# Optimization experiments

Measured on AMD Instinct MI355X. Metric: run time of the kernel, lower is better.

The kernel has to match this reference:

```python
import jax, jax.numpy as jnp
import numpy as np
import math

B, S, D, H = 2, 2048, 1024, 32
HD = D // H  # head_dim = 32
NEG = -1e9


def setup_inputs() -> dict:
    key = jax.random.key(0)
    ks = jax.random.split(key, 6)
    x = jax.random.normal(ks[0], (B, S, D), dtype=jnp.float32)
    # additive causal mask: 0 on/below diagonal, -1e9 above
    causal = jnp.tril(jnp.ones((S, S), dtype=bool))
    mask = jnp.where(causal, 0.0, NEG).astype(jnp.float32)[None, None]
    # SSMax-style per-query-position log-length scale
    section_log_len = jnp.log(jnp.arange(1, S + 1, dtype=jnp.float32) + 1.0).reshape(1, 1, S, 1)
    sc = 1.0 / math.sqrt(D)
    wq = jax.random.normal(ks[1], (D, D), dtype=jnp.float32) * sc
    wk = jax.random.normal(ks[2], (D, D), dtype=jnp.float32) * sc
    wv = jax.random.normal(ks[3], (D, D), dtype=jnp.float32) * sc
    wo = jax.random.normal(ks[4], (D, D), dtype=jnp.float32) * sc
    seq_scale = jnp.ones((1, H, 1, 1), dtype=jnp.float32)
    return {"x": x, "mask": mask, "section_log_len": section_log_len,
            "wq": wq, "wk": wk, "wv": wv, "wo": wo, "seq_scale": seq_scale}


def reference(x, mask, section_log_len, wq, wk, wv, wo, seq_scale):
    bsz, seqlen, dim = x.shape
    # projections (torch Linear: y = x @ W.T); split heads -> [b, h, s, hd]
    q = (x @ wq.T).reshape(bsz, seqlen, H, HD).transpose(0, 2, 1, 3)
    k = (x @ wk.T).reshape(bsz, seqlen, H, HD).transpose(0, 2, 1, 3)
    v = (x @ wv.T).reshape(bsz, seqlen, H, HD).transpose(0, 2, 1, 3)
    # n_kv_heads == n_heads, so repeat_kv is identity
    scores = jnp.einsum('bhqd,bhkd->bhqk', q, k) / math.sqrt(HD)
    scores = scores * (section_log_len * seq_scale)  # SSMax per-head learned scale
    scores = scores + mask
    probs = jax.nn.softmax(scores.astype(jnp.float32), axis=-1).astype(q.dtype)
    out = jnp.einsum('bhqk,bhkd->bhqd', probs, v)
    out = out.transpose(0, 2, 1, 3).reshape(bsz, seqlen, dim)
    return out @ wo.T
```

## Files before the change

### kernel.cpp

```cpp
#include <hip/hip_runtime.h>
#include <hip/hip_bf16.h>

typedef __bf16 bf16_t;
typedef bf16_t bf16x8 __attribute__((ext_vector_type(8)));
typedef float f32x4 __attribute__((ext_vector_type(4)));

#define NB 2
#define SEQ 2048
#define DIM 1024
#define NH 32
#define HDIM 32

#define LDA 40

static __device__ __forceinline__ f32x4 mfma16(bf16x8 a, bf16x8 b, f32x4 c) {
    return __builtin_amdgcn_mfma_f32_16x16x32_bf16(a, b, c, 0, 0, 0);
}

static __device__ __forceinline__ float fexp2(float x) {
    float r;
    asm("v_exp_f32 %0, %1" : "=v"(r) : "v"(x));
    return r;
}

static __device__ __forceinline__ void load_lds16(const bf16_t* g, bf16_t* l) {
    __builtin_amdgcn_global_load_lds(
        (const __attribute__((address_space(1))) void*)(g),
        (__attribute__((address_space(3))) void*)(l), 16, 0, 0);
}

__global__ __launch_bounds__(256)
void cvt_f32_bf16(const float* __restrict__ s0, bf16_t* __restrict__ d0, int n0,
                  const float* __restrict__ s1, bf16_t* __restrict__ d1, int n1,
                  const float* __restrict__ s2, bf16_t* __restrict__ d2, int n2,
                  const float* __restrict__ s3, bf16_t* __restrict__ d3, int n3,
                  const float* __restrict__ s4, bf16_t* __restrict__ d4, int n4) {
    const int stride = gridDim.x * blockDim.x;
    const int tid = blockIdx.x * blockDim.x + threadIdx.x;
    const float* src[5] = {s0, s1, s2, s3, s4};
    bf16_t* dst[5] = {d0, d1, d2, d3, d4};
    const int n[5] = {n0, n1, n2, n3, n4};
#pragma unroll
    for (int r = 0; r < 5; r++) {
        const int nv = n[r] >> 2;
        for (int i = tid; i < nv; i += stride) {
            float4 v = ((const float4*)src[r])[i];
            bf16_t o[4] = {(bf16_t)v.x, (bf16_t)v.y, (bf16_t)v.z, (bf16_t)v.w};
            *(uint2*)(dst[r] + i * 4) = *(const uint2*)o;
        }
    }
}

template <int EPI, int BM>
__global__ __launch_bounds__(256)
void gemm_pipe(const bf16_t* __restrict__ A, const bf16_t* __restrict__ W,
               float* __restrict__ Cf, bf16_t* __restrict__ qb,
               bf16_t* __restrict__ kb, bf16_t* __restrict__ vtb,
               const float* __restrict__ slen, const float* __restrict__ ss) {
    constexpr int MI = BM / 32;
    constexpr int ABUF = BM * 32;
    __shared__ alignas(16) bf16_t As[3 * ABUF];
    __shared__ alignas(16) bf16_t Bs[3 * 4096];
    const int t = threadIdx.x;
    const int lane = t & 63, wave = t >> 6;
    const int lane16 = lane & 15, quad = lane >> 4;
    const int wm = (wave >> 1) * (BM / 2), wn = (wave & 1) * 64;
    const int id = blockIdx.x;
    int m0, n0g;
    if (EPI == 1) {
        const int xcd = id & 7, slot = id >> 3;
        m0 = (xcd + 8 * (slot & 3)) * 128;
        n0g = (slot >> 2) * 128;
    } else {
        const int xcd = id & 7, slot = id >> 3;
        m0 = (xcd + 8 * (slot & 7)) * 64;
        n0g = (slot >> 3) * 128;
    }
    const int tr = t >> 2;
    const int tc = ((t & 3) ^ ((tr >> 1) & 3)) * 8;
    const bf16_t* ga = A + (m0 + tr) * DIM + tc;
    const bf16_t* gb = W + (n0g + tr) * DIM + tc;
    const int rq = (quad ^ ((lane16 >> 1) & 3)) * 8;
    const bool vseg = (EPI == 1) && (n0g >= 2048);

    f32x4 acc[MI][4];
#pragma unroll
    for (int i = 0; i < MI; i++)
#pragma unroll
        for (int j = 0; j < 4; j++) acc[i][j] = f32x4{0.f, 0.f, 0.f, 0.f};

    auto stage = [&](int k0, int buf) {
        bf16_t* a_dst = As + buf * ABUF + (t & 192) * 8;
        bf16_t* b_dst = Bs + buf * 4096 + (t & 192) * 8;
        load_lds16(ga + k0, a_dst);
        if (BM == 128) load_lds16(ga + 64 * DIM + k0, a_dst + 2048);
        load_lds16(gb + k0, b_dst);
        load_lds16(gb + 64 * DIM + k0, b_dst + 2048);
    };
    auto compute = [&](int buf) {
        bf16x8 af[MI], bfr[4];
#pragma unroll
        for (int mi = 0; mi < MI; mi++)
            af[mi] = *(const bf16x8*)(As + buf * ABUF +
                                      (wm + mi * 16 + lane16) * 32 + rq);
#pragma unroll
        for (int ni = 0; ni < 4; ni++)
            bfr[ni] = *(const bf16x8*)(Bs + buf * 4096 +
                                       (wn + ni * 16 + lane16) * 32 + rq);
        if (vseg) {
#pragma unroll
            for (int mi = 0; mi < MI; mi++)
#pragma unroll
                for (int ni = 0; ni < 4; ni++)
                    acc[mi][ni] = mfma16(bfr[ni], af[mi], acc[mi][ni]);
        } else {
#pragma unroll
            for (int mi = 0; mi < MI; mi++)
#pragma unroll
                for (int ni = 0; ni < 4; ni++)
                    acc[mi][ni] = mfma16(af[mi], bfr[ni], acc[mi][ni]);
        }
    };

    stage(0, 0);
    stage(32, 1);
#pragma unroll
    for (int k0 = 0; k0 < DIM; k0 += 32) {
        const int it = k0 >> 5;
        const int cur = it % 3;
        if (k0 + 64 < DIM) {
            stage(k0 + 64, (it + 2) % 3);
            if (BM == 128)
                asm volatile("s_waitcnt vmcnt(8)" ::: "memory");
            else
                asm volatile("s_waitcnt vmcnt(6)" ::: "memory");
        } else if (k0 + 32 < DIM) {
            if (BM == 128)
                asm volatile("s_waitcnt vmcnt(4)" ::: "memory");
            else
                asm volatile("s_waitcnt vmcnt(3)" ::: "memory");
        } else {
            asm volatile("s_waitcnt vmcnt(0)" ::: "memory");
        }
        asm volatile("s_barrier" ::: "memory");
        compute(cur);
        if (k0 + 32 < DIM) {
            asm volatile("s_waitcnt lgkmcnt(0)" ::: "memory");
            asm volatile("s_barrier" ::: "memory");
        }
    }

    if (EPI == 0) {
#pragma unroll
        for (int mi = 0; mi < MI; mi++)
#pragma unroll
            for (int ni = 0; ni < 4; ni++)
#pragma unroll
                for (int r = 0; r < 4; r++) {
                    int row = m0 + wm + mi * 16 + quad * 4 + r;
                    int col = n0g + wn + ni * 16 + lane16;
                    Cf[row * DIM + col] = acc[mi][ni][r];
                }
    } else if (!vseg) {
        const bool isq = (n0g < 1024);
        bf16_t* dst = isq ? qb : kb;
        const int nb = n0g & 1023;
#pragma unroll
        for (int mi = 0; mi < MI; mi++)
#pragma unroll
            for (int ni = 0; ni < 4; ni++) {
                const int h = ((nb + wn) >> 5) + (ni >> 1);
                const float hscale =
                    isq ? ss[h] * (0.17677669529663687f * 1.4426950408889634f)
                        : 0.f;
#pragma unroll
                for (int r = 0; r < 4; r++) {
                    int m = m0 + wm + mi * 16 + quad * 4 + r;
                    int nl = nb + wn + ni * 16 + lane16;
                    int b = m >> 11, s = m & (SEQ - 1);
                    int d = nl & 31;
                    float v = acc[mi][ni][r];
                    if (isq) v *= slen[s] * hscale;
                    dst[(((b * NH + h) << 11) + s) * 32 + d] = (bf16_t)v;
                }
            }
    } else {
        const int nb = n0g & 1023;
#pragma unroll
        for (int mi = 0; mi < MI; mi++)
#pragma unroll
            for (int ni = 0; ni < 4; ni++)
#pragma unroll
                for (int r = 0; r < 4; r++) {
                    int nl = nb + wn + ni * 16 + quad * 4 + r;
                    int m = m0 + wm + mi * 16 + lane16;
                    int b = m >> 11, s = m & (SEQ - 1);
                    int h = nl >> 5, d = nl & 31;
                    vtb[(((b * NH + h) << 5) + d) * SEQ + s] = (bf16_t)acc[mi][ni][r];
                }
    }
}

__global__ __launch_bounds__(256)
void attn_fwd(const bf16_t* __restrict__ q, const bf16_t* __restrict__ k,
              const bf16_t* __restrict__ vt, bf16_t* __restrict__ out) {
    __shared__ alignas(16) bf16_t pscr[4][2][32 * LDA];
    const int t = threadIdx.x;
    const int lane = t & 63, wave = t >> 6;
    const int lane16 = lane & 15, quad = lane >> 4;
    const int gw = blockIdx.x * 4 + wave;
    const int idx = gw & 63;
    const int qt = (idx & 1) ? (63 - (idx >> 1)) : (idx >> 1);
    const int h = (gw >> 6) & (NH - 1);
    const int b = gw >> 11;
    const int q0 = qt * 32;
    const bf16_t* qh = q + (b * NH + h) * SEQ * HDIM;
    const bf16_t* kh = k + (b * NH + h) * SEQ * HDIM;
    const bf16_t* vth = vt + (b * NH + h) * HDIM * SEQ;

    bf16_t* wbase0 = pscr[wave][0] + quad * 4 * LDA + 2 * lane16;
    bf16_t* wbase1 = pscr[wave][1] + quad * 4 * LDA + 2 * lane16;
    const bf16_t* rbase0 = pscr[wave][0] + lane16 * LDA + quad * 8;
    const bf16_t* rbase1 = pscr[wave][1] + lane16 * LDA + quad * 8;

    bf16x8 qf[2];
    qf[0] = *(const bf16x8*)(qh + (q0 + lane16) * HDIM + quad * 8);
    qf[1] = *(const bf16x8*)(qh + (q0 + 16 + lane16) * HDIM + quad * 8);

    bf16x8 ones;
#pragma unroll
    for (int j = 0; j < 8; j++) ones[j] = (bf16_t)1.0f;

    f32x4 o[2][2], ol[2], sc[2][2];
#pragma unroll
    for (int mi = 0; mi < 2; mi++) {
        ol[mi] = f32x4{0.f, 0.f, 0.f, 0.f};
#pragma unroll
        for (int ni = 0; ni < 2; ni++) o[mi][ni] = f32x4{0.f, 0.f, 0.f, 0.f};
    }

    const bf16_t* kp0 = kh + (2 * lane16) * HDIM + quad * 8;
    const bf16_t* vp0 = vth + lane16 * SEQ + quad * 8;
    const bf16_t* vp1 = vth + (16 + lane16) * SEQ + quad * 8;

    const f32x4 zz = f32x4{0.f, 0.f, 0.f, 0.f};
    bf16x8 kc0, kc1, pf0, pf1, vprev0, vprev1;

    auto qk = [&]() {
        __builtin_amdgcn_s_setprio(1);
        sc[0][0] = mfma16(qf[0], kc0, zz);
        sc[0][1] = mfma16(qf[0], kc1, zz);
        sc[1][0] = mfma16(qf[1], kc0, zz);
        sc[1][1] = mfma16(qf[1], kc1, zz);
        __builtin_amdgcn_s_setprio(0);
    };
    auto ldp = [&](const bf16_t* rb) {
        pf0 = *(const bf16x8*)(rb);
        pf1 = *(const bf16x8*)(rb + 16 * LDA);
    };
    auto expw = [&](bf16_t* wb, bool domask) {
#pragma unroll
        for (int mi = 0; mi < 2; mi++)
#pragma unroll
            for (int r = 0; r < 4; r++) {
                float p0 = fexp2(sc[mi][0][r]);
                float p1 = fexp2(sc[mi][1][r]);
                if (domask) {
                    const int rowloc = mi * 16 + quad * 4 + r;
                    if (2 * lane16 > rowloc) p0 = 0.f;
                    if (2 * lane16 + 1 > rowloc) p1 = 0.f;
                }
                bf16_t pb[2] = {(bf16_t)p0, (bf16_t)p1};
                *(unsigned int*)(wb + (mi * 16 + r) * LDA) =
                    *(const unsigned int*)pb;
            }
    };
    auto pv = [&]() {
        __builtin_amdgcn_s_setprio(1);
        o[0][0] = mfma16(pf0, vprev0, o[0][0]);
        o[0][1] = mfma16(pf0, vprev1, o[0][1]);
        o[1][0] = mfma16(pf1, vprev0, o[1][0]);
        o[1][1] = mfma16(pf1, vprev1, o[1][1]);
        ol[0] = mfma16(pf0, ones, ol[0]);
        ol[1] = mfma16(pf1, ones, ol[1]);
        __builtin_amdgcn_s_setprio(0);
    };

    const int nb = qt + 1;

    kc0 = *(const bf16x8*)(kp0);
    kc1 = *(const bf16x8*)(kp0 + HDIM);
    qk();
    vprev0 = *(const bf16x8*)(vp0);
    vprev1 = *(const bf16x8*)(vp1);
    if (nb > 1) {
        kc0 = *(const bf16x8*)(kp0 + 32 * HDIM);
        kc1 = *(const bf16x8*)(kp0 + 32 * HDIM + HDIM);
    }
    expw(wbase0, nb == 1);

    for (int i = 1; i < nb - 1; i++) {
        const int kv = i << 5;
        qk();
        bf16x8 vc0 = *(const bf16x8*)(vp0 + kv);
        bf16x8 vc1 = *(const bf16x8*)(vp1 + kv);
        bf16x8 kn0 = *(const bf16x8*)(kp0 + (kv + 32) * HDIM);
        bf16x8 kn1 = *(const bf16x8*)(kp0 + (kv + 32) * HDIM + HDIM);
        ldp(((i - 1) & 1) ? rbase1 : rbase0);
        expw((i & 1) ? wbase1 : wbase0, false);
        pv();
        kc0 = kn0;
        kc1 = kn1;
        vprev0 = vc0;
        vprev1 = vc1;
    }

    if (nb > 1) {
        const int kv = (nb - 1) << 5;
        qk();
        bf16x8 vc0 = *(const bf16x8*)(vp0 + kv);
        bf16x8 vc1 = *(const bf16x8*)(vp1 + kv);
        ldp(((nb - 2) & 1) ? rbase1 : rbase0);
        expw(((nb - 1) & 1) ? wbase1 : wbase0, true);
        pv();
        vprev0 = vc0;
        vprev1 = vc1;
    }

    ldp(((nb - 1) & 1) ? rbase1 : rbase0);
    pv();

#pragma unroll
    for (int mi = 0; mi < 2; mi++)
#pragma unroll
        for (int r = 0; r < 4; r++) {
            float inv = 1.0f / ol[mi][r];
            int qi = q0 + mi * 16 + quad * 4 + r;
            bf16_t* ob = out + (b * SEQ + qi) * DIM + h * HDIM;
            ob[lane16] = (bf16_t)(o[mi][0][r] * inv);
            ob[16 + lane16] = (bf16_t)(o[mi][1][r] * inv);
        }
}

extern "C" void kernel_launch(void* const* d_in, const int* in_sizes, int n_in,
                              void* d_out, int out_size, void* d_ws, size_t ws_size,
                              hipStream_t stream) {
    const float* x = (const float*)d_in[0];
    const float* slen = (const float*)d_in[2];
    const float* wq = (const float*)d_in[3];
    const float* wk = (const float*)d_in[4];
    const float* wv = (const float*)d_in[5];
    const float* wo = (const float*)d_in[6];
    const float* ss = (const float*)d_in[7];

    const size_t ELEMS = (size_t)NB * SEQ * DIM;
    const size_t WELEMS = (size_t)DIM * DIM;
    bf16_t* xb = (bf16_t*)d_ws;
    bf16_t* abuf = xb;
    bf16_t* wqkvb = xb + ELEMS;
    bf16_t* wob = wqkvb + 3 * WELEMS;
    bf16_t* qbuf = wob + WELEMS;
    bf16_t* vtbuf = qbuf + ELEMS;
    bf16_t* kbuf = (bf16_t*)d_out;

    dim3 blk(256);
    cvt_f32_bf16<<<dim3(1024), blk, 0, stream>>>(
        x, xb, (int)ELEMS, wq, wqkvb, (int)WELEMS, wk, wqkvb + WELEMS,
        (int)WELEMS, wv, wqkvb + 2 * WELEMS, (int)WELEMS, wo, wob, (int)WELEMS);

    gemm_pipe<1, 128><<<dim3(768), blk, 0, stream>>>(
        xb, wqkvb, nullptr, qbuf, kbuf, vtbuf, slen, ss);
    attn_fwd<<<dim3(NB * NH * (SEQ / 32) / 4), blk, 0, stream>>>(
        qbuf, kbuf, vtbuf, abuf);
    gemm_pipe<0, 64><<<dim3(512), blk, 0, stream>>>(
        abuf, wob, (float*)d_out, nullptr, nullptr, nullptr, nullptr, nullptr);
}
```

Measured before the change: 209.6 us.

## Process 64-key blocks per iteration in attention with wider P scratch

Restructures the attention loop to handle 64 keys per iteration instead of 32, loading four K fragments and four V fragments and doing two QK/exp halves before one PV pass. This halves loop iterations and amortizes LDS round-trips and scheduling overhead. The P scratch stride grows to 72 and launch bounds request 4 blocks per CU. The risks are higher register pressure and more wasted masked work on the diagonal block. The software pipeline is also reordered, with PV issued before the next QK.

```diff
diff --git a/kernel.cpp b/kernel.cpp
--- a/kernel.cpp
+++ b/kernel.cpp
@@ -11,7 +11,7 @@
 #define NH 32
 #define HDIM 32
 
-#define LDA 40
+#define LDP 72
 
 static __device__ __forceinline__ f32x4 mfma16(bf16x8 a, bf16x8 b, f32x4 c) {
     return __builtin_amdgcn_mfma_f32_16x16x32_bf16(a, b, c, 0, 0, 0);
@@ -201,10 +201,10 @@
     }
 }
 
-__global__ __launch_bounds__(256)
+__global__ __launch_bounds__(256, 4)
 void attn_fwd(const bf16_t* __restrict__ q, const bf16_t* __restrict__ k,
               const bf16_t* __restrict__ vt, bf16_t* __restrict__ out) {
-    __shared__ alignas(16) bf16_t pscr[4][2][32 * LDA];
+    __shared__ alignas(16) bf16_t pscr[4][2][32 * LDP];
     const int t = threadIdx.x;
     const int lane = t & 63, wave = t >> 6;
     const int lane16 = lane & 15, quad = lane >> 4;
@@ -218,10 +218,10 @@
     const bf16_t* kh = k + (b * NH + h) * SEQ * HDIM;
     const bf16_t* vth = vt + (b * NH + h) * HDIM * SEQ;
 
-    bf16_t* wbase0 = pscr[wave][0] + quad * 4 * LDA + 2 * lane16;
-    bf16_t* wbase1 = pscr[wave][1] + quad * 4 * LDA + 2 * lane16;
-    const bf16_t* rbase0 = pscr[wave][0] + lane16 * LDA + quad * 8;
-    const bf16_t* rbase1 = pscr[wave][1] + lane16 * LDA + quad * 8;
+    bf16_t* wb0 = pscr[wave][0] + quad * 4 * LDP + 4 * lane16;
+    bf16_t* wb1 = pscr[wave][1] + quad * 4 * LDP + 4 * lane16;
+    const bf16_t* rb0 = pscr[wave][0] + lane16 * LDP + quad * 8;
+    const bf16_t* rb1 = pscr[wave][1] + lane16 * LDP + quad * 8;
 
     bf16x8 qf[2];
     qf[0] = *(const bf16x8*)(qh + (q0 + lane16) * HDIM + quad * 8);
@@ -231,7 +231,7 @@
 #pragma unroll
     for (int j = 0; j < 8; j++) ones[j] = (bf16_t)1.0f;
 
-    f32x4 o[2][2], ol[2], sc[2][2];
+    f32x4 o[2][2], ol[2];
 #pragma unroll
     for (int mi = 0; mi < 2; mi++) {
         ol[mi] = f32x4{0.f, 0.f, 0.f, 0.f};
@@ -239,26 +239,24 @@
         for (int ni = 0; ni < 2; ni++) o[mi][ni] = f32x4{0.f, 0.f, 0.f, 0.f};
     }
 
-    const bf16_t* kp0 = kh + (2 * lane16) * HDIM + quad * 8;
-    const bf16_t* vp0 = vth + lane16 * SEQ + quad * 8;
-    const bf16_t* vp1 = vth + (16 + lane16) * SEQ + quad * 8;
+    const bf16_t* kptr = kh + (4 * lane16) * HDIM + quad * 8;
+    const bf16_t* vpa = vth + lane16 * SEQ + quad * 8;
+    const bf16_t* vpb = vth + (16 + lane16) * SEQ + quad * 8;
 
     const f32x4 zz = f32x4{0.f, 0.f, 0.f, 0.f};
-    bf16x8 kc0, kc1, pf0, pf1, vprev0, vprev1;
-
-    auto qk = [&]() {
+    bf16x8 kc[4], vc[4], pf[2][2];
+
+    const int nb64 = (qt >> 1) + 1;
+
+    auto qkexp = [&](int hh, bf16_t* wb, int kv, bool domask) {
+        f32x4 sc[2][2];
         __builtin_amdgcn_s_setprio(1);
-        sc[0][0] = mfma16(qf[0], kc0, zz);
-        sc[0][1] = mfma16(qf[0], kc1, zz);
-        sc[1][0] = mfma16(qf[1], kc0, zz);
-        sc[1][1] = mfma16(qf[1], kc1, zz);
+#pragma unroll
+        for (int mi = 0; mi < 2; mi++)
+#pragma unroll
+            for (int j = 0; j < 2; j++)
+                sc[mi][j] = mfma16(qf[mi], kc[2 * hh + j], zz);
         __builtin_amdgcn_s_setprio(0);
-    };
-    auto ldp = [&](const bf16_t* rb) {
-        pf0 = *(const bf16x8*)(rb);
-        pf1 = *(const bf16x8*)(rb + 16 * LDA);
-    };
-    auto expw = [&](bf16_t* wb, bool domask) {
 #pragma unroll
         for (int mi = 0; mi < 2; mi++)
 #pragma unroll
@@ -266,68 +264,84 @@
                 float p0 = fexp2(sc[mi][0][r]);
                 float p1 = fexp2(sc[mi][1][r]);
                 if (domask) {
-                    const int rowloc = mi * 16 + quad * 4 + r;
-                    if (2 * lane16 > rowloc) p0 = 0.f;
-                    if (2 * lane16 + 1 > rowloc) p1 = 0.f;
+                    const int rowg = q0 + mi * 16 + quad * 4 + r;
+                    if (kv + 4 * lane16 + 2 * hh > rowg) p0 = 0.f;
+                    if (kv + 4 * lane16 + 2 * hh + 1 > rowg) p1 = 0.f;
                 }
                 bf16_t pb[2] = {(bf16_t)p0, (bf16_t)p1};
-                *(unsigned int*)(wb + (mi * 16 + r) * LDA) =
+                *(unsigned int*)(wb + (mi * 16 + r) * LDP + 2 * hh) =
                     *(const unsigned int*)pb;
             }
     };
+    auto ldk = [&]() {
+#pragma unroll
+        for (int tt = 0; tt < 4; tt++) kc[tt] = *(const bf16x8*)(kptr + tt * HDIM);
+        kptr += 64 * HDIM;
+    };
+    auto ldv = [&](int kv) {
+        vc[0] = *(const bf16x8*)(vpa + kv);
+        vc[1] = *(const bf16x8*)(vpa + kv + 32);
+        vc[2] = *(const bf16x8*)(vpb + kv);
+        vc[3] = *(const bf16x8*)(vpb + kv + 32);
+    };
+    auto ldp = [&](const bf16_t* rb) {
+#pragma unroll
+        for (int mi = 0; mi < 2; mi++) {
+            pf[mi][0] = *(const bf16x8*)(rb + mi * 16 * LDP);
+            pf[mi][1] = *(const bf16x8*)(rb + mi * 16 * LDP + 32);
+        }
+    };
     auto pv = [&]() {
         __builtin_amdgcn_s_setprio(1);
-        o[0][0] = mfma16(pf0, vprev0, o[0][0]);
-        o[0][1] = mfma16(pf0, vprev1, o[0][1]);
-        o[1][0] = mfma16(pf1, vprev0, o[1][0]);
-        o[1][1] = mfma16(pf1, vprev1, o[1][1]);
-        ol[0] = mfma16(pf0, ones, ol[0]);
-        ol[1] = mfma16(pf1, ones, ol[1]);
+#pragma unroll
+        for (int mi = 0; mi < 2; mi++) {
+#pragma unroll
+            for (int ni = 0; ni < 2; ni++) {
+                o[mi][ni] = mfma16(pf[mi][0], vc[2 * ni], o[mi][ni]);
+                o[mi][ni] = mfma16(pf[mi][1], vc[2 * ni + 1], o[mi][ni]);
+            }
+            ol[mi] = mfma16(pf[mi][0], ones, ol[mi]);
+            ol[mi] = mfma16(pf[mi][1], ones, ol[mi]);
+        }
         __builtin_amdgcn_s_setprio(0);
     };
 
-    const int nb = qt + 1;
-
-    kc0 = *(const bf16x8*)(kp0);
-    kc1 = *(const bf16x8*)(kp0 + HDIM);
-    qk();
-    vprev0 = *(const bf16x8*)(vp0);
-    vprev1 = *(const bf16x8*)(vp1);
-    if (nb > 1) {
-        kc0 = *(const bf16x8*)(kp0 + 32 * HDIM);
-        kc1 = *(const bf16x8*)(kp0 + 32 * HDIM + HDIM);
-    }
-    expw(wbase0, nb == 1);
-
-    for (int i = 1; i < nb - 1; i++) {
-        const int kv = i << 5;
-        qk();
-        bf16x8 vc0 = *(const bf16x8*)(vp0 + kv);
-        bf16x8 vc1 = *(const bf16x8*)(vp1 + kv);
-        bf16x8 kn0 = *(const bf16x8*)(kp0 + (kv + 32) * HDIM);
-        bf16x8 kn1 = *(const bf16x8*)(kp0 + (kv + 32) * HDIM + HDIM);
-        ldp(((i - 1) & 1) ? rbase1 : rbase0);
-        expw((i & 1) ? wbase1 : wbase0, false);
+    ldk();
+    ldv(0);
+    {
+        const bool m0only = (nb64 == 1);
+        qkexp(0, wb0, 0, m0only);
+        bf16x8 ksave[4];
+        qkexp(1, wb0, 0, m0only);
+        (void)ksave;
+        ldk();
+    }
+
+    for (int i = 1; i < nb64 - 1; i++) {
+        const int kv = i << 6;
+        bf16_t* wb = (i & 1) ? wb1 : wb0;
+        const bf16_t* rb = (i & 1) ? rb0 : rb1;
+        ldp(rb);
         pv();
-        kc0 = kn0;
-        kc1 = kn1;
-        vprev0 = vc0;
-        vprev1 = vc1;
-    }
-
-    if (nb > 1) {
-        const int kv = (nb - 1) << 5;
-        qk();
-        bf16x8 vc0 = *(const bf16x8*)(vp0 + kv);
-        bf16x8 vc1 = *(const bf16x8*)(vp1 + kv);
-        ldp(((nb - 2) & 1) ? rbase1 : rbase0);
-        expw(((nb - 1) & 1) ? wbase1 : wbase0, true);
+        ldv(kv);
+        qkexp(0, wb, kv, false);
+        qkexp(1, wb, kv, false);
+        ldk();
+    }
+
+    if (nb64 > 1) {
+        const int i = nb64 - 1;
+        const int kv = i << 6;
+        bf16_t* wb = (i & 1) ? wb1 : wb0;
+        const bf16_t* rb = (i & 1) ? rb0 : rb1;
+        ldp(rb);
         pv();
-        vprev0 = vc0;
-        vprev1 = vc1;
-    }
-
-    ldp(((nb - 1) & 1) ? rbase1 : rbase0);
+        ldv(kv);
+        qkexp(0, wb, kv, true);
+        qkexp(1, wb, kv, true);
+    }
+
+    ldp(((nb64 - 1) & 1) ? rb1 : rb0);
     pv();
 
 #pragma unroll
```

Result: no change. 210.6 us (+0.5%).
